# Performance work log

Hardware: AMD Instinct MI355X
Metric: run time of the kernel (lower is better)

## Reference

```python
import jax, jax.numpy as jnp
import numpy as np

N, E, S, G = 20000, 60000, 3000, 128
EAD = 5
DIMS = [(16, 32), (32, 64), (64, 64)]  # NNConv (M_in, M_out) per layer
HID = 128  # edge-MLP hidden
FC_IN = 64 + 8  # conv output + raw continuous feats


def setup_inputs() -> dict:
    key = jax.random.key(0)
    ks = iter(jax.random.split(key, 64))
    inp = {}
    inp['x'] = jax.random.normal(next(ks), (N, 24), jnp.float32)
    inp['edge_index'] = jax.random.randint(next(ks), (2, E), 0, N)
    inp['edge_attr'] = jax.random.uniform(next(ks), (E, EAD), jnp.float32)
    inp['node_to_subgraph'] = jnp.sort(jax.random.randint(next(ks), (N,), 0, S))
    inp['subgraph_to_graph'] = jnp.sort(jax.random.randint(next(ks), (S,), 0, G))
    for i, (mi, mo) in enumerate(DIMS):
        inp[f'conv{i}_w1'] = jax.random.normal(next(ks), (EAD, HID), jnp.float32) / np.sqrt(EAD)
        inp[f'conv{i}_b1'] = jnp.zeros((HID,), jnp.float32)
        inp[f'conv{i}_w2'] = jax.random.normal(next(ks), (HID, mi * mo), jnp.float32) / np.sqrt(HID * mi)
        inp[f'conv{i}_b2'] = jnp.zeros((mi * mo,), jnp.float32)
        inp[f'conv{i}_root'] = jax.random.normal(next(ks), (mi, mo), jnp.float32) / np.sqrt(mi)
        inp[f'conv{i}_bias'] = jnp.zeros((mo,), jnp.float32)
    dims_fc = [(FC_IN, FC_IN // 2), (FC_IN // 2, FC_IN // 4), (FC_IN // 4, 1)]
    for i, (di, do) in enumerate(dims_fc):
        inp[f'fc{i+1}_w'] = jax.random.normal(next(ks), (di, do), jnp.float32) / np.sqrt(di)
        inp[f'fc{i+1}_b'] = jnp.zeros((do,), jnp.float32)
    return inp


def _nnconv(x, src, dst, ea, w1, b1, w2, b2, root, bias):
    # edge MLP -> per-edge weight matrix [E, M_in, M_out]
    h = jax.nn.relu(ea @ w1 + b1)
    mi, mo = root.shape
    W = (h @ w2 + b2).reshape(-1, mi, mo)
    msg = jnp.einsum('ei,eio->eo', x[src], W)  # gather + per-edge matmul
    agg = jax.ops.segment_sum(msg, dst, num_segments=x.shape[0])  # scatter-add
    return agg + x @ root + bias


def _mean_pool(x, seg, num):
    s = jax.ops.segment_sum(x, seg, num_segments=num)
    c = jax.ops.segment_sum(jnp.ones((x.shape[0], 1), x.dtype), seg, num_segments=num)
    return s / jnp.maximum(c, 1.0)


def _forward(x, edge_index, edge_attr, node_to_subgraph, subgraph_to_graph, convs, fcs):
    src, dst = edge_index[0], edge_index[1]
    xi = x[:, :16]
    for p in convs:
        xi = jax.nn.elu(_nnconv(xi, src, dst, edge_attr, *p))
    x_cont = x[:, 16:]
    xc = jnp.concatenate([xi, x_cont], axis=1)  # [N, 72]
    xs = _mean_pool(xc, node_to_subgraph, S)    # [S, 72]
    xg = _mean_pool(xs, subgraph_to_graph, G)   # [G, 72]
    (w1, b1), (w2, b2), (w3, b3) = fcs
    xg = jax.nn.elu(xg @ w1 + b1)
    xg = jax.nn.elu(xg @ w2 + b2)
    return (xg @ w3 + b3).reshape(-1)


def reference(x, edge_index, edge_attr, node_to_subgraph, subgraph_to_graph,
              conv0_w1, conv0_b1, conv0_w2, conv0_b2, conv0_root, conv0_bias,
              conv1_w1, conv1_b1, conv1_w2, conv1_b2, conv1_root, conv1_bias,
              conv2_w1, conv2_b1, conv2_w2, conv2_b2, conv2_root, conv2_bias,
              fc1_w, fc1_b, fc2_w, fc2_b, fc3_w, fc3_b):
    convs = [
        (conv0_w1, conv0_b1, conv0_w2, conv0_b2, conv0_root, conv0_bias),
        (conv1_w1, conv1_b1, conv1_w2, conv1_b2, conv1_root, conv1_bias),
        (conv2_w1, conv2_b1, conv2_w2, conv2_b2, conv2_root, conv2_bias),
    ]
    fcs = [(fc1_w, fc1_b), (fc2_w, fc2_b), (fc3_w, fc3_b)]
    return _forward(x, edge_index, edge_attr, node_to_subgraph, subgraph_to_graph, convs, fcs)
```

## Files before the change

### kernel.cpp

```cpp
#include <hip/hip_runtime.h>
#include <hip/hip_bf16.h>
#include <cmath>

#define NN 20000
#define NE 60000
#define NS 3000
#define NG 128
#define HIDN 128
#define SCB 79

typedef float f32x16 __attribute__((ext_vector_type(16)));
typedef _Float16 f16x8 __attribute__((ext_vector_type(8)));

__device__ __forceinline__ float eluf(float v) { return v > 0.f ? v : expm1f(v); }

__device__ __forceinline__ void gload_lds16(const void* g, void* l) {
    __builtin_amdgcn_global_load_lds(
        (const __attribute__((address_space(1))) unsigned int*)g,
        (__attribute__((address_space(3))) unsigned int*)l, 16, 0, 0);
}

__device__ __forceinline__ void vmwait0() {
    asm volatile("s_waitcnt vmcnt(0)" ::: "memory");
}

__global__ void k_hist(const int* __restrict__ dst, int* __restrict__ deg) {
    int e = blockIdx.x * 256 + threadIdx.x;
    if (e < NE) atomicAdd(&deg[dst[e]], 1);
}

__global__ void k_scan1(const int* __restrict__ deg, int* __restrict__ bsum) {
    __shared__ int s[256];
    const int t = threadIdx.x;
    int i = blockIdx.x * 256 + t;
    s[t] = (i < NN) ? deg[i] : 0;
    __syncthreads();
#pragma unroll
    for (int off = 128; off > 0; off >>= 1) {
        if (t < off) s[t] += s[t + off];
        __syncthreads();
    }
    if (t == 0) bsum[blockIdx.x] = s[0];
}

__global__ void k_scan2(const int* __restrict__ bsum, int* __restrict__ boff) {
    __shared__ int s[SCB];
    const int t = threadIdx.x;
    if (t < SCB) s[t] = bsum[t];
    __syncthreads();
    if (t == 0) {
        int acc = 0;
        for (int i = 0; i < SCB; ++i) { int v = s[i]; s[i] = acc; acc += v; }
    }
    __syncthreads();
    if (t < SCB) boff[t] = s[t];
}

__global__ void k_scan3(const int* __restrict__ deg, const int* __restrict__ boff,
                        int* __restrict__ rowptr) {
    __shared__ int s[256];
    const int t = threadIdx.x;
    int i = blockIdx.x * 256 + t;
    int v = (i < NN) ? deg[i] : 0;
    s[t] = v;
    __syncthreads();
#pragma unroll
    for (int off = 1; off < 256; off <<= 1) {
        int a = (t >= off) ? s[t - off] : 0;
        __syncthreads();
        s[t] += a;
        __syncthreads();
    }
    if (i < NN) rowptr[i + 1] = boff[blockIdx.x] + s[t];
    if (i == 0) rowptr[0] = 0;
}

__global__ void k_scatter(const int* __restrict__ src, const int* __restrict__ dst,
                          const int* __restrict__ rowptr, int* __restrict__ tmp,
                          int* __restrict__ eord, int* __restrict__ srcS) {
    int e = blockIdx.x * 256 + threadIdx.x;
    if (e >= NE) return;
    int d = dst[e];
    int pos = rowptr[d] + atomicAdd(&tmp[d], 1);
    eord[pos] = e;
    srcS[pos] = src[e];
}

template <int MI, int MO>
__global__ void k_w2t(const float* __restrict__ w2, const float* __restrict__ b2,
                      _Float16* __restrict__ w2t) {
    constexpr int KP = 129 * MI;
    constexpr int KF = 128 * MI;
    int idx = blockIdx.x * 256 + threadIdx.x;
    if (idx >= MO * KP) return;
    int o = idx / KP, kg = idx % KP;
    float v = (kg < KF) ? w2[(size_t)kg * MO + o] : b2[(kg - KF) * MO + o];
    w2t[idx] = (_Float16)v;
}

__global__ void k_x16h(const float* __restrict__ x, _Float16* __restrict__ xh) {
    int idx = blockIdx.x * 256 + threadIdx.x;
    if (idx >= NN * 16) return;
    int n = idx >> 4, i = idx & 15;
    xh[idx] = (_Float16)x[n * 24 + i];
}

template <int MI, int MO, int XS>
__global__ __launch_bounds__(256, 2) void k_edge9(
    const _Float16* __restrict__ xi, const float* __restrict__ ea,
    const float* __restrict__ w1, const float* __restrict__ b1,
    const _Float16* __restrict__ w2t, const int* __restrict__ srcS,
    const int* __restrict__ eord, float* __restrict__ msg) {
    constexpr int PH  = MI / 16;
    constexpr int KP  = 129 * MI;
    constexpr int NT  = MO / 32;
    constexpr int CH  = 16 / (PH * NT);
    constexpr int NCH = 64 / CH;
    static_assert(CH * PH * NT == 16, "ITEMS must be 16");
    static_assert(NCH % 2 == 0, "chunk loop unrolled x2");

    __shared__ __align__(16) _Float16 sb[2][2][16 * 512];

    const int lane = threadIdx.x & 63;
    const int w    = threadIdx.x >> 6;
    const int mg   = w & 1;
    const int kh   = w >> 1;
    const int lo5  = lane & 31;
    const int hi   = lane >> 5;
    const int e0   = blockIdx.x * 128 + mg * 64;
    const int kb   = kh * 64;

    const int rc0 = min(e0 + lo5, NE - 1);
    const int rc1 = min(e0 + 32 + lo5, NE - 1);
    const int s0 = srcS[rc0];
    const int s1 = srcS[rc1];

    float ea0[5], ea1[5];
    {
        const int eo0 = eord[rc0], eo1 = eord[rc1];
#pragma unroll
        for (int d = 0; d < 5; ++d) {
            ea0[d] = ea[eo0 * 5 + d];
            ea1[d] = ea[eo1 * 5 + d];
        }
    }

    f16x8 xr0[PH], xr1[PH];
    {
        const _Float16* xb0 = xi + (size_t)s0 * XS + hi * 8;
        const _Float16* xb1 = xi + (size_t)s1 * XS + hi * 8;
#pragma unroll
        for (int p = 0; p < PH; ++p) {
            xr0[p] = *reinterpret_cast<const f16x8*>(xb0 + p * 16);
            xr1[p] = *reinterpret_cast<const f16x8*>(xb1 + p * 16);
        }
    }

    f32x16 acc[2][NT];
#pragma unroll
    for (int m = 0; m < 2; ++m)
#pragma unroll
        for (int n = 0; n < NT; ++n)
#pragma unroll
            for (int i = 0; i < 16; ++i) acc[m][n][i] = 0.f;

    auto stage = [&](int buf, int kc) {
#pragma unroll
        for (int jj = 0; jj < 8; ++jj) {
            const int j  = mg + jj * 2;
            const int n  = j % NT;
            const int kp = j / NT;
            const int p  = kp % PH;
            const int kk = kp / PH;
            gload_lds16(w2t + (size_t)(n * 32 + lo5) * KP
                            + (size_t)(kb + kc + kk) * MI + p * 16 + hi * 8,
                        &sb[kh][buf][j * 512]);
        }
    };

    auto calc_h = [&](int kc, _Float16* h0, _Float16* h1) {
#pragma unroll
        for (int kk = 0; kk < CH; ++kk) {
            const int k = kb + kc + kk;
            const float c0 = w1[0 * HIDN + k], c1 = w1[1 * HIDN + k],
                        c2 = w1[2 * HIDN + k], c3 = w1[3 * HIDN + k],
                        c4 = w1[4 * HIDN + k], bb = b1[k];
            float t0 = bb, t1 = bb;
            t0 = fmaf(ea0[0], c0, t0); t1 = fmaf(ea1[0], c0, t1);
            t0 = fmaf(ea0[1], c1, t0); t1 = fmaf(ea1[1], c1, t1);
            t0 = fmaf(ea0[2], c2, t0); t1 = fmaf(ea1[2], c2, t1);
            t0 = fmaf(ea0[3], c3, t0); t1 = fmaf(ea1[3], c3, t1);
            t0 = fmaf(ea0[4], c4, t0); t1 = fmaf(ea1[4], c4, t1);
            h0[kk] = (_Float16)fmaxf(t0, 0.f);
            h1[kk] = (_Float16)fmaxf(t1, 0.f);
        }
    };

    auto compute = [&](int buf, const _Float16* h0, const _Float16* h1) {
        const _Float16* sbc = &sb[kh][buf][0];
#pragma unroll
        for (int kk = 0; kk < CH; ++kk) {
            const _Float16 hv0 = h0[kk];
            const _Float16 hv1 = h1[kk];
            const f16x8 h80 = {hv0, hv0, hv0, hv0, hv0, hv0, hv0, hv0};
            const f16x8 h81 = {hv1, hv1, hv1, hv1, hv1, hv1, hv1, hv1};
#pragma unroll
            for (int p = 0; p < PH; ++p) {
                const f16x8 af0 = xr0[p] * h80;
                const f16x8 af1 = xr1[p] * h81;
#pragma unroll
                for (int n = 0; n < NT; ++n) {
                    const f16x8 bv = *reinterpret_cast<const f16x8*>(
                        &sbc[((kk * PH + p) * NT + n) * 512 + lane * 8]);
                    acc[0][n] = __builtin_amdgcn_mfma_f32_32x32x16_f16(af0, bv, acc[0][n], 0, 0, 0);
                    acc[1][n] = __builtin_amdgcn_mfma_f32_32x32x16_f16(af1, bv, acc[1][n], 0, 0, 0);
                }
            }
        }
    };

    _Float16 hA0[CH], hA1[CH], hB0[CH], hB1[CH];

    stage(0, 0);
    calc_h(0, hA0, hA1);

    for (int c = 0; c < NCH; c += 2) {
        vmwait0();
        __builtin_amdgcn_sched_barrier(0);
        __builtin_amdgcn_s_barrier();
        __builtin_amdgcn_sched_barrier(0);
        stage(1, (c + 1) * CH);
        calc_h((c + 1) * CH, hB0, hB1);
        compute(0, hA0, hA1);
        __builtin_amdgcn_sched_barrier(0);

        vmwait0();
        __builtin_amdgcn_sched_barrier(0);
        __builtin_amdgcn_s_barrier();
        __builtin_amdgcn_sched_barrier(0);
        const bool pf = (c + 2 < NCH);
        if (pf) {
            stage(0, (c + 2) * CH);
            calc_h((c + 2) * CH, hA0, hA1);
        }
        compute(1, hB0, hB1);
        __builtin_amdgcn_sched_barrier(0);
    }

    if (kh == 1) {
#pragma unroll
        for (int p = 0; p < PH; ++p) {
#pragma unroll
            for (int n = 0; n < NT; ++n) {
                const f16x8 bv = *reinterpret_cast<const f16x8*>(
                    w2t + (size_t)(n * 32 + lo5) * KP + (size_t)128 * MI + p * 16 + hi * 8);
                acc[0][n] = __builtin_amdgcn_mfma_f32_32x32x16_f16(xr0[p], bv, acc[0][n], 0, 0, 0);
                acc[1][n] = __builtin_amdgcn_mfma_f32_32x32x16_f16(xr1[p], bv, acc[1][n], 0, 0, 0);
            }
        }
    }

    __syncthreads();
    float* red = reinterpret_cast<float*>(&sb[0][0][0]);
    if (kh == 1) {
#pragma unroll
        for (int m = 0; m < 2; ++m)
#pragma unroll
            for (int n = 0; n < NT; ++n) {
                float* d = red + (size_t)((mg * 2 + m) * NT + n) * 1024 + lane;
#pragma unroll
                for (int i = 0; i < 16; ++i) d[i * 64] = acc[m][n][i];
            }
    }
    __syncthreads();
    if (kh == 0) {
#pragma unroll
        for (int m = 0; m < 2; ++m)
#pragma unroll
            for (int n = 0; n < NT; ++n) {
                const float* s = red + (size_t)((mg * 2 + m) * NT + n) * 1024 + lane;
#pragma unroll
                for (int i = 0; i < 16; ++i) acc[m][n][i] += s[i * 64];
            }
#pragma unroll
        for (int m = 0; m < 2; ++m)
#pragma unroll
            for (int q = 0; q < 4; ++q)
#pragma unroll
                for (int a2 = 0; a2 < 4; ++a2) {
                    const int e = e0 + m * 32 + 4 * hi + 8 * q + a2;
                    if (e < NE) {
#pragma unroll
                        for (int n = 0; n < NT; ++n)
                            msg[(size_t)e * MO + n * 32 + lo5] = acc[m][n][4 * q + a2];
                    }
                }
    }
}

template <int MI, int MO, int XS>
__global__ void k_agg(const float* __restrict__ msg, const int* __restrict__ rowptr,
                      const float* __restrict__ xi, const float* __restrict__ root,
                      const float* __restrict__ bias, float* __restrict__ out,
                      _Float16* __restrict__ outh) {
    int idx = blockIdx.x * 256 + threadIdx.x;
    if (idx >= NN * MO) return;
    int n = idx / MO, o = idx % MO;
    float s = bias[o];
#pragma unroll
    for (int i = 0; i < MI; ++i) s = fmaf(xi[(size_t)n * XS + i], root[i * MO + o], s);
    const int j0 = rowptr[n], j1 = rowptr[n + 1];
    for (int j = j0; j < j1; ++j) s += msg[(size_t)j * MO + o];
    float r = eluf(s);
    out[idx] = r;
    outh[idx] = (_Float16)r;
}

__global__ void k_pool_s(const float* __restrict__ xi, const float* __restrict__ x,
                         const int* __restrict__ n2s, float* __restrict__ xs_sum,
                         float* __restrict__ cs) {
    int idx = blockIdx.x * 256 + threadIdx.x;
    if (idx >= NN * 72) return;
    int n = idx / 72, j = idx % 72;
    float v = (j < 64) ? xi[n * 64 + j] : x[n * 24 + 16 + (j - 64)];
    int s = n2s[n];
    atomicAdd(&xs_sum[s * 72 + j], v);
    if (j == 0) atomicAdd(&cs[s], 1.f);
}

__global__ void k_pool_g(const float* __restrict__ xs_sum, const float* __restrict__ cs,
                         const int* __restrict__ s2g, float* __restrict__ xg_sum,
                         float* __restrict__ cg) {
    int idx = blockIdx.x * 256 + threadIdx.x;
    if (idx >= NS * 72) return;
    int s = idx / 72, j = idx % 72;
    float v = xs_sum[s * 72 + j] / fmaxf(cs[s], 1.f);
    int g = s2g[s];
    atomicAdd(&xg_sum[g * 72 + j], v);
    if (j == 0) atomicAdd(&cg[g], 1.f);
}

__global__ void k_fc(const float* __restrict__ xg_sum, const float* __restrict__ cg,
                     const float* __restrict__ w1, const float* __restrict__ b1,
                     const float* __restrict__ w2, const float* __restrict__ b2,
                     const float* __restrict__ w3, const float* __restrict__ b3,
                     float* __restrict__ out) {
    int g = threadIdx.x;
    if (g >= NG) return;
    float inv = 1.f / fmaxf(cg[g], 1.f);
    float v[72];
#pragma unroll
    for (int j = 0; j < 72; ++j) v[j] = xg_sum[g * 72 + j] * inv;
    float h1[36];
#pragma unroll
    for (int o = 0; o < 36; ++o) {
        float s = b1[o];
#pragma unroll
        for (int i = 0; i < 72; ++i) s = fmaf(v[i], w1[i * 36 + o], s);
        h1[o] = eluf(s);
    }
    float h2[18];
#pragma unroll
    for (int o = 0; o < 18; ++o) {
        float s = b2[o];
#pragma unroll
        for (int i = 0; i < 36; ++i) s = fmaf(h1[i], w2[i * 18 + o], s);
        h2[o] = eluf(s);
    }
    float s = b3[0];
#pragma unroll
    for (int i = 0; i < 18; ++i) s = fmaf(h2[i], w3[i], s);
    out[g] = s;
}

extern "C" void kernel_launch(void* const* d_in, const int* in_sizes, int n_in,
                              void* d_out, int out_size, void* d_ws, size_t ws_size,
                              hipStream_t stream) {
    const float* x   = (const float*)d_in[0];
    const int*   ei  = (const int*)d_in[1];
    const float* ea  = (const float*)d_in[2];
    const int*   n2s = (const int*)d_in[3];
    const int*   s2g = (const int*)d_in[4];
    const int* src = ei;
    const int* dst = ei + NE;

    const float* cw1[3]   = {(const float*)d_in[5],  (const float*)d_in[11], (const float*)d_in[17]};
    const float* cb1[3]   = {(const float*)d_in[6],  (const float*)d_in[12], (const float*)d_in[18]};
    const float* cw2[3]   = {(const float*)d_in[7],  (const float*)d_in[13], (const float*)d_in[19]};
    const float* cb2[3]   = {(const float*)d_in[8],  (const float*)d_in[14], (const float*)d_in[20]};
    const float* croot[3] = {(const float*)d_in[9],  (const float*)d_in[15], (const float*)d_in[21]};
    const float* cbias[3] = {(const float*)d_in[10], (const float*)d_in[16], (const float*)d_in[22]};
    const float* fc1w = (const float*)d_in[23];
    const float* fc1b = (const float*)d_in[24];
    const float* fc2w = (const float*)d_in[25];
    const float* fc2b = (const float*)d_in[26];
    const float* fc3w = (const float*)d_in[27];
    const float* fc3b = (const float*)d_in[28];

    char* W = (char*)d_ws;
    float*    xiA   = (float*)(W);
    float*    xiB   = (float*)(W + 5120000);
    _Float16* xiAh  = (_Float16*)(W + 10240000);
    _Float16* xiBh  = (_Float16*)(W + 12800000);
    _Float16* x16h  = (_Float16*)(W + 15360000);
    float*    msg   = (float*)(W + 16000000);
    float*    xs_sum= (float*)(W + 31360000);
    float*    cs    = (float*)(W + 32224000);
    float*    xg_sum= (float*)(W + 32236000);
    float*    cg    = (float*)(W + 32272864);
    _Float16* w2t0  = (_Float16*)(W + 32273376);
    _Float16* w2t1  = (_Float16*)(W + 32405472);
    _Float16* w2t2  = (_Float16*)(W + 32933856);
    int*      deg   = (int*)(W + 33990624);
    int*      tmp   = (int*)(W + 34070624);
    int*      rowptr= (int*)(W + 34150624);
    int*      eord  = (int*)(W + 34230640);
    int*      srcS  = (int*)(W + 34470640);
    int*      bsum  = (int*)(W + 34710640);
    int*      boff  = (int*)(W + 34710960);

    hipMemsetAsync(xs_sum, 0, (size_t)(NS * 72 + NS) * 4 + (size_t)(NG * 72 + NG) * 4, stream);
    hipMemsetAsync(deg, 0, 160000, stream);

    k_hist<<<(NE + 255) / 256, 256, 0, stream>>>(dst, deg);
    k_scan1<<<SCB, 256, 0, stream>>>(deg, bsum);
    k_scan2<<<1, 128, 0, stream>>>(bsum, boff);
    k_scan3<<<SCB, 256, 0, stream>>>(deg, boff, rowptr);
    k_scatter<<<(NE + 255) / 256, 256, 0, stream>>>(src, dst, rowptr, tmp, eord, srcS);

    k_w2t<16, 32><<<(32 * 129 * 16 + 255) / 256, 256, 0, stream>>>(cw2[0], cb2[0], w2t0);
    k_w2t<32, 64><<<(64 * 129 * 32 + 255) / 256, 256, 0, stream>>>(cw2[1], cb2[1], w2t1);
    k_w2t<64, 64><<<(64 * 129 * 64 + 255) / 256, 256, 0, stream>>>(cw2[2], cb2[2], w2t2);
    k_x16h<<<(NN * 16 + 255) / 256, 256, 0, stream>>>(x, x16h);

    const int EB = (NE + 127) / 128;

    k_edge9<16, 32, 16><<<EB, 256, 0, stream>>>(x16h, ea, cw1[0], cb1[0], w2t0, srcS, eord, msg);
    k_agg<16, 32, 24><<<(NN * 32 + 255) / 256, 256, 0, stream>>>(msg, rowptr, x, croot[0], cbias[0], xiB, xiBh);

    k_edge9<32, 64, 32><<<EB, 256, 0, stream>>>(xiBh, ea, cw1[1], cb1[1], w2t1, srcS, eord, msg);
    k_agg<32, 64, 32><<<(NN * 64 + 255) / 256, 256, 0, stream>>>(msg, rowptr, xiB, croot[1], cbias[1], xiA, xiAh);

    k_edge9<64, 64, 64><<<EB, 256, 0, stream>>>(xiAh, ea, cw1[2], cb1[2], w2t2, srcS, eord, msg);
    k_agg<64, 64, 64><<<(NN * 64 + 255) / 256, 256, 0, stream>>>(msg, rowptr, xiA, croot[2], cbias[2], xiB, xiBh);

    k_pool_s<<<(NN * 72 + 255) / 256, 256, 0, stream>>>(xiB, x, n2s, xs_sum, cs);
    k_pool_g<<<(NS * 72 + 255) / 256, 256, 0, stream>>>(xs_sum, cs, s2g, xg_sum, cg);
    k_fc<<<1, 128, 0, stream>>>(xg_sum, cg, fc1w, fc1b, fc2w, fc2b, fc3w, fc3b, (float*)d_out);
}
```

Measured before the change: 307.9 us.

## Split edge-kernel output columns across a second grid dimension

The per-edge NNConv kernel now handles a single 32-wide output tile per block and sends the output-column tiles along blockIdx.y. Layers with 64 outputs therefore launch twice as many blocks, each holding half the accumulators and running a chunk loop with more k steps per stage. The aim is more parallelism and fewer live registers. The cost is that each y-block recomputes the edge-MLP hidden values and reloads the gathered x rows and edge attributes.

```diff
diff --git a/kernel.cpp b/kernel.cpp
--- a/kernel.cpp
+++ b/kernel.cpp
@@ -106,17 +106,16 @@
 }
 
 template <int MI, int MO, int XS>
-__global__ __launch_bounds__(256, 2) void k_edge9(
+__global__ __launch_bounds__(256, 2) void k_edgeA(
     const _Float16* __restrict__ xi, const float* __restrict__ ea,
     const float* __restrict__ w1, const float* __restrict__ b1,
     const _Float16* __restrict__ w2t, const int* __restrict__ srcS,
     const int* __restrict__ eord, float* __restrict__ msg) {
     constexpr int PH  = MI / 16;
     constexpr int KP  = 129 * MI;
-    constexpr int NT  = MO / 32;
-    constexpr int CH  = 16 / (PH * NT);
+    constexpr int CH  = 16 / PH;
     constexpr int NCH = 64 / CH;
-    static_assert(CH * PH * NT == 16, "ITEMS must be 16");
+    static_assert(CH * PH == 16, "ITEMS must be 16");
     static_assert(NCH % 2 == 0, "chunk loop unrolled x2");
 
     __shared__ __align__(16) _Float16 sb[2][2][16 * 512];
@@ -128,6 +127,7 @@
     const int lo5  = lane & 31;
     const int hi   = lane >> 5;
     const int e0   = blockIdx.x * 128 + mg * 64;
+    const int ns   = blockIdx.y;
     const int kb   = kh * 64;
 
     const int rc0 = min(e0 + lo5, NE - 1);
@@ -156,24 +156,19 @@
         }
     }
 
-    f32x16 acc[2][NT];
-#pragma unroll
-    for (int m = 0; m < 2; ++m)
-#pragma unroll
-        for (int n = 0; n < NT; ++n)
-#pragma unroll
-            for (int i = 0; i < 16; ++i) acc[m][n][i] = 0.f;
+    f32x16 acc0, acc1;
+#pragma unroll
+    for (int i = 0; i < 16; ++i) { acc0[i] = 0.f; acc1[i] = 0.f; }
+
+    const _Float16* bbase = w2t + (size_t)(ns * 32 + lo5) * KP + hi * 8;
 
     auto stage = [&](int buf, int kc) {
 #pragma unroll
         for (int jj = 0; jj < 8; ++jj) {
             const int j  = mg + jj * 2;
-            const int n  = j % NT;
-            const int kp = j / NT;
-            const int p  = kp % PH;
-            const int kk = kp / PH;
-            gload_lds16(w2t + (size_t)(n * 32 + lo5) * KP
-                            + (size_t)(kb + kc + kk) * MI + p * 16 + hi * 8,
+            const int kk = j / PH;
+            const int p  = j % PH;
+            gload_lds16(bbase + (size_t)(kb + kc + kk) * MI + p * 16,
                         &sb[kh][buf][j * 512]);
         }
     };
@@ -208,18 +203,15 @@
             for (int p = 0; p < PH; ++p) {
                 const f16x8 af0 = xr0[p] * h80;
                 const f16x8 af1 = xr1[p] * h81;
-#pragma unroll
-                for (int n = 0; n < NT; ++n) {
-                    const f16x8 bv = *reinterpret_cast<const f16x8*>(
-                        &sbc[((kk * PH + p) * NT + n) * 512 + lane * 8]);
-                    acc[0][n] = __builtin_amdgcn_mfma_f32_32x32x16_f16(af0, bv, acc[0][n], 0, 0, 0);
-                    acc[1][n] = __builtin_amdgcn_mfma_f32_32x32x16_f16(af1, bv, acc[1][n], 0, 0, 0);
-                }
+                const f16x8 bv = *reinterpret_cast<const f16x8*>(
+                    &sbc[(kk * PH + p) * 512 + lane * 8]);
+                acc0 = __builtin_amdgcn_mfma_f32_32x32x16_f16(af0, bv, acc0, 0, 0, 0);
+                acc1 = __builtin_amdgcn_mfma_f32_32x32x16_f16(af1, bv, acc1, 0, 0, 0);
             }
         }
     };
 
-    _Float16 hA0[CH], hA1[CH], hB0[CH], hB1[CH];
+    _Float16 hA0[16], hA1[16], hB0[16], hB1[16];
 
     stage(0, 0);
     calc_h(0, hA0, hA1);
@@ -250,13 +242,10 @@
     if (kh == 1) {
 #pragma unroll
         for (int p = 0; p < PH; ++p) {
-#pragma unroll
-            for (int n = 0; n < NT; ++n) {
-                const f16x8 bv = *reinterpret_cast<const f16x8*>(
-                    w2t + (size_t)(n * 32 + lo5) * KP + (size_t)128 * MI + p * 16 + hi * 8);
-                acc[0][n] = __builtin_amdgcn_mfma_f32_32x32x16_f16(xr0[p], bv, acc[0][n], 0, 0, 0);
-                acc[1][n] = __builtin_amdgcn_mfma_f32_32x32x16_f16(xr1[p], bv, acc[1][n], 0, 0, 0);
-            }
+            const f16x8 bv = *reinterpret_cast<const f16x8*>(
+                bbase + (size_t)128 * MI + p * 16);
+            acc0 = __builtin_amdgcn_mfma_f32_32x32x16_f16(xr0[p], bv, acc0, 0, 0, 0);
+            acc1 = __builtin_amdgcn_mfma_f32_32x32x16_f16(xr1[p], bv, acc1, 0, 0, 0);
         }
     }
 
@@ -264,24 +253,22 @@
     float* red = reinterpret_cast<float*>(&sb[0][0][0]);
     if (kh == 1) {
 #pragma unroll
-        for (int m = 0; m < 2; ++m)
-#pragma unroll
-            for (int n = 0; n < NT; ++n) {
-                float* d = red + (size_t)((mg * 2 + m) * NT + n) * 1024 + lane;
-#pragma unroll
-                for (int i = 0; i < 16; ++i) d[i * 64] = acc[m][n][i];
-            }
+        for (int m = 0; m < 2; ++m) {
+            float* d = red + (size_t)(mg * 2 + m) * 1024 + lane;
+            const f32x16& a = (m == 0) ? acc0 : acc1;
+#pragma unroll
+            for (int i = 0; i < 16; ++i) d[i * 64] = a[i];
+        }
     }
     __syncthreads();
     if (kh == 0) {
 #pragma unroll
-        for (int m = 0; m < 2; ++m)
-#pragma unroll
-            for (int n = 0; n < NT; ++n) {
-                const float* s = red + (size_t)((mg * 2 + m) * NT + n) * 1024 + lane;
-#pragma unroll
-                for (int i = 0; i < 16; ++i) acc[m][n][i] += s[i * 64];
-            }
+        for (int m = 0; m < 2; ++m) {
+            const float* s = red + (size_t)(mg * 2 + m) * 1024 + lane;
+            f32x16& a = (m == 0) ? acc0 : acc1;
+#pragma unroll
+            for (int i = 0; i < 16; ++i) a[i] += s[i * 64];
+        }
 #pragma unroll
         for (int m = 0; m < 2; ++m)
 #pragma unroll
@@ -290,9 +277,8 @@
                 for (int a2 = 0; a2 < 4; ++a2) {
                     const int e = e0 + m * 32 + 4 * hi + 8 * q + a2;
                     if (e < NE) {
-#pragma unroll
-                        for (int n = 0; n < NT; ++n)
-                            msg[(size_t)e * MO + n * 32 + lo5] = acc[m][n][4 * q + a2];
+                        const float v = (m == 0) ? acc0[4 * q + a2] : acc1[4 * q + a2];
+                        msg[(size_t)e * MO + ns * 32 + lo5] = v;
                     }
                 }
     }
@@ -435,13 +421,13 @@
 
     const int EB = (NE + 127) / 128;
 
-    k_edge9<16, 32, 16><<<EB, 256, 0, stream>>>(x16h, ea, cw1[0], cb1[0], w2t0, srcS, eord, msg);
+    k_edgeA<16, 32, 16><<<dim3(EB, 1), 256, 0, stream>>>(x16h, ea, cw1[0], cb1[0], w2t0, srcS, eord, msg);
     k_agg<16, 32, 24><<<(NN * 32 + 255) / 256, 256, 0, stream>>>(msg, rowptr, x, croot[0], cbias[0], xiB, xiBh);
 
-    k_edge9<32, 64, 32><<<EB, 256, 0, stream>>>(xiBh, ea, cw1[1], cb1[1], w2t1, srcS, eord, msg);
+    k_edgeA<32, 64, 32><<<dim3(EB, 2), 256, 0, stream>>>(xiBh, ea, cw1[1], cb1[1], w2t1, srcS, eord, msg);
     k_agg<32, 64, 32><<<(NN * 64 + 255) / 256, 256, 0, stream>>>(msg, rowptr, xiB, croot[1], cbias[1], xiA, xiAh);
 
-    k_edge9<64, 64, 64><<<EB, 256, 0, stream>>>(xiAh, ea, cw1[2], cb1[2], w2t2, srcS, eord, msg);
+    k_edgeA<64, 64, 64><<<dim3(EB, 2), 256, 0, stream>>>(xiAh, ea, cw1[2], cb1[2], w2t2, srcS, eord, msg);
     k_agg<64, 64, 64><<<(NN * 64 + 255) / 256, 256, 0, stream>>>(msg, rowptr, xiA, croot[2], cbias[2], xiB, xiBh);
 
     k_pool_s<<<(NN * 72 + 255) / 256, 256, 0, stream>>>(xiB, x, n2s, xs_sum, cs);
```

After: 314.0 us. About the same (+2.0%).
